# Optimization experiments

Hardware: AMD Instinct MI355X
Metric: run time of the kernel (lower is better)

The kernel has to match this reference:

```python
import jax, jax.numpy as jnp
import numpy as np

D_IN = 1024
D_OUT = 1024
NUM_HEADS = 16
HEAD_DIM = D_OUT // NUM_HEADS


def setup_inputs() -> dict:
    key = jax.random.key(0)
    k_x, k_q, k_k, k_v, k_o, k_ob = jax.random.split(key, 6)
    s_in = 1.0 / np.sqrt(D_IN)
    s_out = 1.0 / np.sqrt(D_OUT)
    return {
        "x": jax.random.normal(k_x, (4, 2048, D_IN), dtype=jnp.float32),
        "W_Q": jax.random.uniform(k_q, (D_IN, D_OUT), jnp.float32, -s_in, s_in),
        "W_K": jax.random.uniform(k_k, (D_IN, D_OUT), jnp.float32, -s_in, s_in),
        "W_V": jax.random.uniform(k_v, (D_IN, D_OUT), jnp.float32, -s_in, s_in),
        "W_O": jax.random.uniform(k_o, (D_OUT, D_OUT), jnp.float32, -s_out, s_out),
        "b_O": jax.random.uniform(k_ob, (D_OUT,), jnp.float32, -s_out, s_out),
    }


def reference(x, W_Q, W_K, W_V, W_O, b_O):
    B, T, _ = x.shape
    # projections -> [B, H, T, Dh]
    Q = (x @ W_Q).reshape(B, T, NUM_HEADS, HEAD_DIM).transpose(0, 2, 1, 3)
    K = (x @ W_K).reshape(B, T, NUM_HEADS, HEAD_DIM).transpose(0, 2, 1, 3)
    V = (x @ W_V).reshape(B, T, NUM_HEADS, HEAD_DIM).transpose(0, 2, 1, 3)
    scores = jnp.einsum("bhqd,bhkd->bhqk", Q, K) / np.sqrt(HEAD_DIM).astype(np.float32)
    causal = jnp.tril(jnp.ones((T, T), dtype=bool))  # True = keep
    scores = jnp.where(causal, scores, -jnp.inf)
    weights = jax.nn.softmax(scores, axis=-1)
    ctx = jnp.einsum("bhqk,bhkd->bhqd", weights, V)
    ctx = ctx.transpose(0, 2, 1, 3).reshape(B, T, D_OUT)
    return ctx @ W_O + b_O
```

## Files before the change

### kernel.cpp

```cpp
#include <hip/hip_runtime.h>

typedef unsigned short ushort_t;
typedef __attribute__((ext_vector_type(8))) __bf16 bf16x8;
typedef __attribute__((ext_vector_type(4))) float f32x4;
typedef __attribute__((ext_vector_type(16))) float f32x16;
typedef __attribute__((ext_vector_type(4))) unsigned short us4;
typedef __attribute__((ext_vector_type(8))) unsigned short us8;
typedef __attribute__((ext_vector_type(4))) unsigned int u32x4;

#define AS1 __attribute__((address_space(1)))
#define AS3 __attribute__((address_space(3)))

__device__ __forceinline__ unsigned short f2bf(float f) {
    unsigned u = __float_as_uint(f);
    u += 0x7fff + ((u >> 16) & 1);
    return (unsigned short)(u >> 16);
}

__device__ __forceinline__ unsigned cvtpk_bf16(float lo, float hi) {
    unsigned r;
    asm("v_cvt_pk_bf16_f32 %0, %1, %2" : "=v"(r) : "v"(lo), "v"(hi));
    return r;
}

__device__ __forceinline__ float fast_exp2(float x) {
    float r;
    asm("v_exp_f32 %0, %1" : "=v"(r) : "v"(x));
    return r;
}

__global__ void k_convert_x(const float* __restrict__ x, ushort_t* __restrict__ xb, int n4) {
    int i = blockIdx.x * blockDim.x + threadIdx.x;
    int stride = gridDim.x * blockDim.x;
    for (; i < n4; i += stride) {
        float4 f = reinterpret_cast<const float4*>(x)[i];
        us4 o = { f2bf(f.x), f2bf(f.y), f2bf(f.z), f2bf(f.w) };
        reinterpret_cast<us4*>(xb)[i] = o;
    }
}

__global__ void k_transpose_w(const float* __restrict__ wq, const float* __restrict__ wk,
                              const float* __restrict__ wv, const float* __restrict__ wo,
                              ushort_t* __restrict__ wqkvt, ushort_t* __restrict__ wot) {
    __shared__ float t[64][65];
    int bx = blockIdx.x;
    int w = bx >> 8;
    int ti = bx & 255;
    int k0 = (ti >> 4) * 64, n0 = (ti & 15) * 64;
    const float* src = (w == 0) ? wq : (w == 1) ? wk : (w == 2) ? wv : wo;
    ushort_t* dst = (w < 3) ? (wqkvt + (size_t)w * 1048576) : wot;
    for (int i = threadIdx.x; i < 4096; i += 256) {
        int r = i >> 6, c = i & 63;
        t[c][r] = src[(size_t)(k0 + r) * 1024 + n0 + c];
    }
    __syncthreads();
    for (int i = threadIdx.x; i < 4096; i += 256) {
        int r = i >> 6, c = i & 63;
        dst[(size_t)(n0 + r) * 1024 + k0 + c] = f2bf(t[r][c]);
    }
}

__global__ __launch_bounds__(512, 2) void k_gemm_qkv256(
    const ushort_t* __restrict__ A, const ushort_t* __restrict__ Bm,
    ushort_t* __restrict__ qd, ushort_t* __restrict__ kd, ushort_t* __restrict__ vd) {
    __shared__ __attribute__((aligned(16))) ushort_t lds[2 * 28672];

    const int tid = threadIdx.x, wid = tid >> 6, lane = tid & 63;
    const int lr = lane & 15, lg = lane >> 4;
    const int wm = wid >> 2, wn = wid & 3;

    int bid = blockIdx.x;
    int wg = (bid & 7) * 64 + (bid >> 3);
    const int by = wg >> 4, bx = wg & 15;
    const int row0 = by * 256, col0 = bx * 192;

    const int srcrow = lane >> 2;
    const int srccol = (((lane & 3) * 16) ^ ((lane >> 5) << 5)) >> 1;
    const ushort_t* aS = A  + (size_t)(row0 + srcrow) * 1024 + srccol;
    const ushort_t* bS = Bm + (size_t)(col0 + srcrow) * 1024 + srccol;
    const int rdoff = (lr * 64 + lg * 16) ^ ((lr >> 3) << 5);

    const int s0 = (wid & 3) + ((wid >> 2) << 3);
    const int s1 = s0 + 4;
    const int bmix_sr = 8 + (wid & 3);
    const int bmix_sc = wid >> 2;

#define STG_A(kt, sr, sc) \
    __builtin_amdgcn_global_load_lds((const AS1 void*)(aS + (size_t)(sr) * 16384 + (kt) * 64 + (sc) * 32), \
        (AS3 void*)((AS3 char*)lds + ((kt) & 1) * 57344 + (sr) * 2048 + (sc) * 1024), 16, 0, 0)
#define STG_B(kt, sr, sc) \
    __builtin_amdgcn_global_load_lds((const AS1 void*)(bS + (size_t)(sr) * 16384 + (kt) * 64 + (sc) * 32), \
        (AS3 void*)((AS3 char*)lds + ((kt) & 1) * 57344 + 32768 + (sr) * 2048 + (sc) * 1024), 16, 0, 0)
#define GRP1(kt)  { STG_A(kt, s0, 0); STG_B(kt, wid, 0); }
#define GRP2(kt)  { STG_A(kt, s1, 0); }
#define GRP3(kt)  { STG_A(kt, s0, 1); STG_B(kt, wid, 1); }
#define GTOP(kt)  { STG_A(kt, s1, 1); STG_B(kt, bmix_sr, bmix_sc); }

    f32x4 acc[8][3] = {};

    GRP1(0); GRP2(0); GRP3(0); GTOP(0);
    GRP1(1); GRP2(1); GRP3(1);

#pragma unroll 1
    for (int kt = 0; kt < 16; ++kt) {
        if (kt < 15) asm volatile("s_waitcnt vmcnt(5)" ::: "memory");
        else         asm volatile("s_waitcnt vmcnt(0)" ::: "memory");
        __builtin_amdgcn_s_barrier();
        if (kt < 15) GTOP(kt + 1);

        const char* bufA = (const char*)lds + (kt & 1) * 57344;
        const char* bufB = bufA + 32768;

        bf16x8 av0[4], av1[4], bv0[3], bv1[3];
#pragma unroll
        for (int x = 0; x < 4; ++x)
            av0[x] = *reinterpret_cast<const bf16x8*>(bufA + (wm * 8 + x) * 2048 + rdoff);
#pragma unroll
        for (int x = 0; x < 3; ++x)
            bv0[x] = *reinterpret_cast<const bf16x8*>(bufB + (wn * 3 + x) * 2048 + rdoff);

#pragma unroll
        for (int x = 0; x < 4; ++x)
            av1[x] = *reinterpret_cast<const bf16x8*>(bufA + (wm * 8 + 4 + x) * 2048 + rdoff);
        __builtin_amdgcn_s_setprio(1);
#pragma unroll
        for (int mf = 0; mf < 4; ++mf)
#pragma unroll
            for (int nf = 0; nf < 3; ++nf)
                acc[mf][nf] = __builtin_amdgcn_mfma_f32_16x16x32_bf16(av0[mf], bv0[nf], acc[mf][nf], 0, 0, 0);
        __builtin_amdgcn_s_setprio(0);
        __builtin_amdgcn_s_barrier();

#pragma unroll
        for (int x = 0; x < 4; ++x)
            av0[x] = *reinterpret_cast<const bf16x8*>(bufA + (wm * 8 + x) * 2048 + 1024 + rdoff);
#pragma unroll
        for (int x = 0; x < 3; ++x)
            bv1[x] = *reinterpret_cast<const bf16x8*>(bufB + (wn * 3 + x) * 2048 + 1024 + rdoff);
        __builtin_amdgcn_s_setprio(1);
#pragma unroll
        for (int mf = 0; mf < 4; ++mf)
#pragma unroll
            for (int nf = 0; nf < 3; ++nf)
                acc[4 + mf][nf] = __builtin_amdgcn_mfma_f32_16x16x32_bf16(av1[mf], bv0[nf], acc[4 + mf][nf], 0, 0, 0);
        __builtin_amdgcn_s_setprio(0);
        if (kt < 14) GRP1(kt + 2);
        __builtin_amdgcn_s_barrier();

#pragma unroll
        for (int x = 0; x < 4; ++x)
            av1[x] = *reinterpret_cast<const bf16x8*>(bufA + (wm * 8 + 4 + x) * 2048 + 1024 + rdoff);
        __builtin_amdgcn_s_setprio(1);
#pragma unroll
        for (int mf = 0; mf < 4; ++mf)
#pragma unroll
            for (int nf = 0; nf < 3; ++nf)
                acc[mf][nf] = __builtin_amdgcn_mfma_f32_16x16x32_bf16(av0[mf], bv1[nf], acc[mf][nf], 0, 0, 0);
        __builtin_amdgcn_s_setprio(0);
        if (kt < 14) GRP2(kt + 2);
        __builtin_amdgcn_s_barrier();

        __builtin_amdgcn_s_setprio(1);
#pragma unroll
        for (int mf = 0; mf < 4; ++mf)
#pragma unroll
            for (int nf = 0; nf < 3; ++nf)
                acc[4 + mf][nf] = __builtin_amdgcn_mfma_f32_16x16x32_bf16(av1[mf], bv1[nf], acc[4 + mf][nf], 0, 0, 0);
        __builtin_amdgcn_s_setprio(0);
        if (kt < 14) GRP3(kt + 2);
    }
#undef STG_A
#undef STG_B
#undef GRP1
#undef GRP2
#undef GRP3
#undef GTOP

#pragma unroll
    for (int mi = 0; mi < 8; ++mi) {
#pragma unroll
        for (int nf = 0; nf < 3; ++nf) {
            int col = col0 + wn * 48 + nf * 16 + lr;
            int w = col >> 10;
            int c1 = col & 1023;
            int h = c1 >> 6, dh = c1 & 63;
            ushort_t* dst = (w == 0) ? qd : (w == 1) ? kd : vd;
            const float osc = (w == 0) ? 0.18033688f : 1.0f;
#pragma unroll
            for (int e = 0; e < 4; ++e) {
                int row = row0 + wm * 128 + mi * 16 + lg * 4 + e;
                int b = row >> 11, t = row & 2047;
                dst[(((size_t)(b * 16 + h)) * 2048 + t) * 64 + dh] = f2bf(acc[mi][nf][e] * osc);
            }
        }
    }
}

__global__ __launch_bounds__(256) void k_transpose_v(const ushort_t* __restrict__ vd,
                                                     ushort_t* __restrict__ vt) {
    __shared__ __attribute__((aligned(16))) ushort_t tile[64 * 72];
    int bid = blockIdx.x;
    int bh = bid >> 5, tt = bid & 31;
    const ushort_t* src = vd + ((size_t)bh * 2048 + tt * 64) * 64;
    ushort_t* dst = vt + (size_t)bh * 2048 * 64 + tt * 64;
#pragma unroll
    for (int r = 0; r < 2; ++r) {
        int i = r * 256 + threadIdx.x;
        int t = i >> 3, c8 = (i & 7) * 8;
        us8 v = *reinterpret_cast<const us8*>(src + (size_t)t * 64 + c8);
        *reinterpret_cast<us8*>(&tile[t * 72 + (c8 ^ ((t >> 3) << 3))]) = v;
    }
    __syncthreads();
#pragma unroll
    for (int r = 0; r < 2; ++r) {
        int i = r * 256 + threadIdx.x;
        int dh = i >> 3, t8 = (i & 7) * 8;
        us8 o;
#pragma unroll
        for (int e = 0; e < 8; ++e)
            o[e] = tile[(t8 + e) * 72 + (dh ^ ((t8 >> 3) << 3))];
        *reinterpret_cast<us8*>(dst + (size_t)dh * 2048 + t8) = o;
    }
}

__global__ __launch_bounds__(256) void k_attn(
    const ushort_t* __restrict__ q, const ushort_t* __restrict__ k,
    const ushort_t* __restrict__ v, ushort_t* __restrict__ ctx) {
    __shared__ __attribute__((aligned(16))) ushort_t lsK[2 * 8192];
    __shared__ __attribute__((aligned(16))) ushort_t lsV[2 * 8192];

    const int tid = threadIdx.x, wid = tid >> 6, lane = tid & 63;
    const int l31 = lane & 31, hi = lane >> 5;
    const int bid = blockIdx.x;
    const int bh = bid >> 3, pi = bid & 7;
    const size_t base = (size_t)bh * 2048 * 64;
    const ushort_t* qg = q + base;
    const ushort_t* kg = k + base;
    const ushort_t* vtg = v + base;
    const int b = bh >> 4, h = bh & 15;

    const int skey = wid * 8 + (lane >> 3);
    const int scb0 = ((lane & 7) * 16) ^ ((skey & 7) << 4);
    const int kx = (l31 & 7) << 4;
    int koffA[4];
#pragma unroll
    for (int s = 0; s < 4; ++s)
        koffA[s] = l31 * 128 + ((s * 32 + hi * 16) ^ kx);

    us8 ow;
#pragma unroll
    for (int e = 0; e < 8; ++e) ow[e] = 0x3F80;
    const bf16x8 onef = __builtin_bit_cast(bf16x8, ow);

#pragma unroll 1
    for (int pass = 0; pass < 2; ++pass) {
        const int qt = pass ? pi : (15 - pi);
        const int q0 = qt * 128;
        const int q0w = q0 + wid * 32;
        const int qrow = q0w + l31;
        const int njt = qt + 1;

        bf16x8 qf[4];
#pragma unroll
        for (int s = 0; s < 4; ++s)
            qf[s] = *reinterpret_cast<const bf16x8*>(qg + (size_t)qrow * 64 + s * 16 + hi * 8);

        const ushort_t* kpr[4];
        const ushort_t* vpr[4];
#pragma unroll
        for (int r = 0; r < 4; ++r) {
            kpr[r] = kg + (size_t)(r * 32 + skey) * 64 + (scb0 >> 1);
            vpr[r] = vtg + (size_t)((r & 1) * 32 + skey) * 2048 + (r >> 1) * 64 + (scb0 >> 1);
        }

        f32x16 acc0 = {}, acc1 = {}, lacc = {};

        __syncthreads();
#pragma unroll
        for (int r = 0; r < 4; ++r) {
            __builtin_amdgcn_global_load_lds((const AS1 void*)kpr[r],
                (AS3 void*)((AS3 char*)lsK + r * 4096 + wid * 1024), 16, 0, 0);
            __builtin_amdgcn_global_load_lds((const AS1 void*)vpr[r],
                (AS3 void*)((AS3 char*)lsV + r * 4096 + wid * 1024), 16, 0, 0);
        }

        unsigned bo = 0;
        for (int jt = 0; jt < njt; ++jt) {
            __syncthreads();
            const int j0 = jt << 7;
            if (jt + 1 < njt) {
                const unsigned nb = bo ^ 16384;
#pragma unroll
                for (int r = 0; r < 4; ++r) {
                    kpr[r] += 8192;
                    vpr[r] += 128;
                    __builtin_amdgcn_global_load_lds((const AS1 void*)kpr[r],
                        (AS3 void*)((AS3 char*)lsK + nb + r * 4096 + wid * 1024), 16, 0, 0);
                    __builtin_amdgcn_global_load_lds((const AS1 void*)vpr[r],
                        (AS3 void*)((AS3 char*)lsV + nb + r * 4096 + wid * 1024), 16, 0, 0);
                }
            }

#pragma unroll
            for (int hh = 0; hh < 2; ++hh) {
                const int j0h = j0 + hh * 64;
                if (j0h < q0w + 32) {
                    const char* bK = reinterpret_cast<const char*>(lsK) + bo + hh * 8192;
                    const char* bV = reinterpret_cast<const char*>(lsV) + bo + hh * 8192;

                    f32x16 s0 = {}, s1 = {};
#pragma unroll
                    for (int s = 0; s < 4; ++s) {
                        bf16x8 ka = *reinterpret_cast<const bf16x8*>(bK + koffA[s]);
                        s0 = __builtin_amdgcn_mfma_f32_32x32x16_bf16(ka, qf[s], s0, 0, 0, 0);
                    }
#pragma unroll
                    for (int s = 0; s < 4; ++s) {
                        bf16x8 ka = *reinterpret_cast<const bf16x8*>(bK + 4096 + koffA[s]);
                        s1 = __builtin_amdgcn_mfma_f32_32x32x16_bf16(ka, qf[s], s1, 0, 0, 0);
                    }

                    float p0[16], p1[16];
                    if (j0h + 63 > q0w) {
                        const int jh = j0h + 4 * hi;
#pragma unroll
                        for (int r = 0; r < 16; ++r) {
                            const int kl = jh + (r & 3) + 8 * (r >> 2);
                            float e0 = fast_exp2(s0[r]);
                            float e1 = fast_exp2(s1[r]);
                            p0[r] = (kl > qrow) ? 0.f : e0;
                            p1[r] = (kl + 32 > qrow) ? 0.f : e1;
                        }
                    } else {
#pragma unroll
                        for (int r = 0; r < 16; ++r) {
                            p0[r] = fast_exp2(s0[r]);
                            p1[r] = fast_exp2(s1[r]);
                        }
                    }

#pragma unroll
                    for (int kb = 0; kb < 2; ++kb) {
                        const float* pp = kb ? p1 : p0;
                        unsigned pw[8];
#pragma unroll
                        for (int g = 0; g < 4; ++g) {
                            pw[2 * g]     = cvtpk_bf16(pp[4 * g],     pp[4 * g + 1]);
                            pw[2 * g + 1] = cvtpk_bf16(pp[4 * g + 2], pp[4 * g + 3]);
                        }
#pragma unroll
                        for (int j = 0; j < 2; ++j) {
                            asm("v_permlane32_swap_b32 %0, %1" : "+v"(pw[4 * j]),     "+v"(pw[4 * j + 2]));
                            asm("v_permlane32_swap_b32 %0, %1" : "+v"(pw[4 * j + 1]), "+v"(pw[4 * j + 3]));
                            u32x4 fw = { pw[4 * j], pw[4 * j + 1], pw[4 * j + 2], pw[4 * j + 3] };
                            bf16x8 pf = __builtin_bit_cast(bf16x8, fw);
                            const int jj = kb * 2 + j;
                            {
                                bf16x8 vf = *reinterpret_cast<const bf16x8*>(bV + koffA[jj]);
                                acc0 = __builtin_amdgcn_mfma_f32_32x32x16_bf16(vf, pf, acc0, 0, 0, 0);
                            }
                            {
                                bf16x8 vf = *reinterpret_cast<const bf16x8*>(bV + 4096 + koffA[jj]);
                                acc1 = __builtin_amdgcn_mfma_f32_32x32x16_bf16(vf, pf, acc1, 0, 0, 0);
                            }
                            lacc = __builtin_amdgcn_mfma_f32_32x32x16_bf16(onef, pf, lacc, 0, 0, 0);
                        }
                    }
                }
            }
            bo ^= 16384;
        }

        float inv = 1.0f / lacc[0];
        size_t orow = ((size_t)(b * 2048 + qrow)) * 1024 + h * 64;
#pragma unroll
        for (int g = 0; g < 4; ++g) {
            us4 o0 = { f2bf(acc0[4 * g] * inv),     f2bf(acc0[4 * g + 1] * inv),
                       f2bf(acc0[4 * g + 2] * inv), f2bf(acc0[4 * g + 3] * inv) };
            *reinterpret_cast<us4*>(&ctx[orow + 8 * g + 4 * hi]) = o0;
            us4 o1 = { f2bf(acc1[4 * g] * inv),     f2bf(acc1[4 * g + 1] * inv),
                       f2bf(acc1[4 * g + 2] * inv), f2bf(acc1[4 * g + 3] * inv) };
            *reinterpret_cast<us4*>(&ctx[orow + 32 + 8 * g + 4 * hi]) = o1;
        }
    }
}

__global__ __launch_bounds__(256) void k_gemm_out(
    const ushort_t* __restrict__ cb, const ushort_t* __restrict__ wot,
    const float* __restrict__ bO, float* __restrict__ out) {
    __shared__ ushort_t lA[128 * 32];
    __shared__ ushort_t lB[128 * 32];
    const int tid = threadIdx.x, wid = tid >> 6, lane = tid & 63;
    const int lr = lane & 15, lg = lane >> 4;
    const int wm = wid >> 1, wn = wid & 1;
    const int bx = blockIdx.x;
    const int by = blockIdx.y;
    const int row0 = by * 128, col0 = bx * 128;
    const int crow = lane >> 2;
    const int coff = (lane & 3) * 8;

    f32x4 acc[4][4] = {};

    for (int k0 = 0; k0 < 1024; k0 += 32) {
        for (int c = wid; c < 8; c += 4) {
            const ushort_t* ga = cb + (size_t)(row0 + c * 16 + crow) * 1024 + k0 + coff;
            __builtin_amdgcn_global_load_lds((const AS1 void*)ga, (AS3 void*)(lA + c * 512), 16, 0, 0);
            const ushort_t* gb = wot + (size_t)(col0 + c * 16 + crow) * 1024 + k0 + coff;
            __builtin_amdgcn_global_load_lds((const AS1 void*)gb, (AS3 void*)(lB + c * 512), 16, 0, 0);
        }
        __syncthreads();
        bf16x8 af[4], bfr[4];
#pragma unroll
        for (int i = 0; i < 4; ++i) {
            af[i]  = *reinterpret_cast<const bf16x8*>(lA + (wm * 64 + i * 16 + lr) * 32 + lg * 8);
            bfr[i] = *reinterpret_cast<const bf16x8*>(lB + (wn * 64 + i * 16 + lr) * 32 + lg * 8);
        }
#pragma unroll
        for (int mi = 0; mi < 4; ++mi)
#pragma unroll
            for (int ni = 0; ni < 4; ++ni)
                acc[mi][ni] = __builtin_amdgcn_mfma_f32_16x16x32_bf16(af[mi], bfr[ni], acc[mi][ni], 0, 0, 0);
        __syncthreads();
    }

#pragma unroll
    for (int mi = 0; mi < 4; ++mi) {
#pragma unroll
        for (int ni = 0; ni < 4; ++ni) {
            int col = col0 + wn * 64 + ni * 16 + lr;
            float bias = bO[col];
#pragma unroll
            for (int e = 0; e < 4; ++e) {
                int row = row0 + wm * 64 + mi * 16 + lg * 4 + e;
                out[(size_t)row * 1024 + col] = acc[mi][ni][e] + bias;
            }
        }
    }
}

extern "C" void kernel_launch(void* const* d_in, const int* in_sizes, int n_in,
                              void* d_out, int out_size, void* d_ws, size_t ws_size,
                              hipStream_t stream) {
    const float* x  = (const float*)d_in[0];
    const float* wq = (const float*)d_in[1];
    const float* wk = (const float*)d_in[2];
    const float* wv = (const float*)d_in[3];
    const float* wo = (const float*)d_in[4];
    const float* bo = (const float*)d_in[5];
    float* out = (float*)d_out;

    char* ws = (char*)d_ws;
    ushort_t* xb    = (ushort_t*)(ws);
    ushort_t* wqkvt = (ushort_t*)(ws + 16777216);
    ushort_t* wot   = (ushort_t*)(ws + 23068672);
    ushort_t* qd    = (ushort_t*)(ws + 25165824);
    ushort_t* kd    = (ushort_t*)(ws + 41943040);
    ushort_t* vd    = (ushort_t*)(ws + 58720256);
    ushort_t* cd    = (ushort_t*)(ws + 75497472);
    ushort_t* vt    = xb;

    k_convert_x<<<2048, 256, 0, stream>>>(x, xb, 8192 * 1024 / 4);
    k_transpose_w<<<1024, 256, 0, stream>>>(wq, wk, wv, wo, wqkvt, wot);
    k_gemm_qkv256<<<512, 512, 0, stream>>>(xb, wqkvt, qd, kd, vd);
    k_transpose_v<<<2048, 256, 0, stream>>>(vd, vt);
    k_attn<<<512, 256, 0, stream>>>(qd, kd, vt, cd);
    k_gemm_out<<<dim3(8, 64), 256, 0, stream>>>(cd, wot, bo, out);
}
```

Before: 168.7 us.

## Pipeline output GEMM with double-buffered swizzled LDS and remap attention block order

Rewrites the output projection GEMM to use a K-tile of 64 with double-buffered LDS, staged global-to-LDS prefetches two tiles ahead, XOR-swizzled LDS layout, and interleaved barriers with MFMA priority bumps. It also remaps the 1D grid so neighbouring blocks share weight columns. Separately, attention blocks are reordered so consecutive blocks cover different heads rather than different query chunks of the same head, which changes load balance for the causal workload. The aim is to hide global-load latency and cut bank conflicts, at the cost of more LDS per block and more complex wait-count bookkeeping.

```diff
diff --git a/kernel.cpp b/kernel.cpp
--- a/kernel.cpp
+++ b/kernel.cpp
@@ -232,7 +232,7 @@
     const int tid = threadIdx.x, wid = tid >> 6, lane = tid & 63;
     const int l31 = lane & 31, hi = lane >> 5;
     const int bid = blockIdx.x;
-    const int bh = bid >> 3, pi = bid & 7;
+    const int bh = bid & 63, pi = bid >> 6;
     const size_t base = (size_t)bh * 2048 * 64;
     const ushort_t* qg = q + base;
     const ushort_t* kg = k + base;
@@ -385,54 +385,120 @@
     }
 }
 
-__global__ __launch_bounds__(256) void k_gemm_out(
+__global__ __launch_bounds__(256, 2) void k_gemm_out(
     const ushort_t* __restrict__ cb, const ushort_t* __restrict__ wot,
     const float* __restrict__ bO, float* __restrict__ out) {
-    __shared__ ushort_t lA[128 * 32];
-    __shared__ ushort_t lB[128 * 32];
+    __shared__ __attribute__((aligned(16))) ushort_t lds[2 * 16384];
+
     const int tid = threadIdx.x, wid = tid >> 6, lane = tid & 63;
     const int lr = lane & 15, lg = lane >> 4;
     const int wm = wid >> 1, wn = wid & 1;
-    const int bx = blockIdx.x;
-    const int by = blockIdx.y;
+
+    int bid = blockIdx.x;
+    int wg = (bid & 7) * 64 + (bid >> 3);
+    const int by = wg >> 3, bx = wg & 7;
     const int row0 = by * 128, col0 = bx * 128;
-    const int crow = lane >> 2;
-    const int coff = (lane & 3) * 8;
+
+    const int srcrow = lane >> 2;
+    const int srccol = (((lane & 3) * 16) ^ ((lane >> 5) << 5)) >> 1;
+    const ushort_t* aS = cb  + (size_t)(row0 + srcrow) * 1024 + srccol;
+    const ushort_t* bS = wot + (size_t)(col0 + srcrow) * 1024 + srccol;
+    const int rdoff = (lr * 64 + lg * 16) ^ ((lr >> 3) << 5);
+
+#define STG_A(kt, sr, sc) \
+    __builtin_amdgcn_global_load_lds((const AS1 void*)(aS + (size_t)(sr) * 16384 + (kt) * 64 + (sc) * 32), \
+        (AS3 void*)((AS3 char*)lds + ((kt) & 1) * 32768 + (sr) * 2048 + (sc) * 1024), 16, 0, 0)
+#define STG_B(kt, sr, sc) \
+    __builtin_amdgcn_global_load_lds((const AS1 void*)(bS + (size_t)(sr) * 16384 + (kt) * 64 + (sc) * 32), \
+        (AS3 void*)((AS3 char*)lds + ((kt) & 1) * 32768 + 16384 + (sr) * 2048 + (sc) * 1024), 16, 0, 0)
+#define GRP1(kt)  { STG_A(kt, wid, 0); STG_A(kt, wid + 4, 0); STG_B(kt, wid, 0); STG_B(kt, wid + 4, 0); }
+#define GTOP(kt)  { STG_A(kt, wid, 1); STG_A(kt, wid + 4, 1); STG_B(kt, wid, 1); STG_B(kt, wid + 4, 1); }
 
     f32x4 acc[4][4] = {};
 
-    for (int k0 = 0; k0 < 1024; k0 += 32) {
-        for (int c = wid; c < 8; c += 4) {
-            const ushort_t* ga = cb + (size_t)(row0 + c * 16 + crow) * 1024 + k0 + coff;
-            __builtin_amdgcn_global_load_lds((const AS1 void*)ga, (AS3 void*)(lA + c * 512), 16, 0, 0);
-            const ushort_t* gb = wot + (size_t)(col0 + c * 16 + crow) * 1024 + k0 + coff;
-            __builtin_amdgcn_global_load_lds((const AS1 void*)gb, (AS3 void*)(lB + c * 512), 16, 0, 0);
-        }
-        __syncthreads();
-        bf16x8 af[4], bfr[4];
-#pragma unroll
-        for (int i = 0; i < 4; ++i) {
-            af[i]  = *reinterpret_cast<const bf16x8*>(lA + (wm * 64 + i * 16 + lr) * 32 + lg * 8);
-            bfr[i] = *reinterpret_cast<const bf16x8*>(lB + (wn * 64 + i * 16 + lr) * 32 + lg * 8);
-        }
-#pragma unroll
-        for (int mi = 0; mi < 4; ++mi)
-#pragma unroll
-            for (int ni = 0; ni < 4; ++ni)
-                acc[mi][ni] = __builtin_amdgcn_mfma_f32_16x16x32_bf16(af[mi], bfr[ni], acc[mi][ni], 0, 0, 0);
-        __syncthreads();
-    }
-
-#pragma unroll
-    for (int mi = 0; mi < 4; ++mi) {
-#pragma unroll
-        for (int ni = 0; ni < 4; ++ni) {
-            int col = col0 + wn * 64 + ni * 16 + lr;
+    GRP1(0); GTOP(0); GRP1(1);
+
+#pragma unroll 1
+    for (int kt = 0; kt < 16; ++kt) {
+        if (kt < 15) asm volatile("s_waitcnt vmcnt(4)" ::: "memory");
+        else         asm volatile("s_waitcnt vmcnt(0)" ::: "memory");
+        __builtin_amdgcn_s_barrier();
+        if (kt < 15) GTOP(kt + 1);
+
+        const char* bufA = (const char*)lds + (kt & 1) * 32768;
+        const char* bufB = bufA + 16384;
+
+        bf16x8 av0[2], av1[2], bv0[4], bv1[4];
+#pragma unroll
+        for (int x = 0; x < 2; ++x)
+            av0[x] = *reinterpret_cast<const bf16x8*>(bufA + (wm * 4 + x) * 2048 + rdoff);
+#pragma unroll
+        for (int x = 0; x < 4; ++x)
+            bv0[x] = *reinterpret_cast<const bf16x8*>(bufB + (wn * 4 + x) * 2048 + rdoff);
+
+#pragma unroll
+        for (int x = 0; x < 2; ++x)
+            av1[x] = *reinterpret_cast<const bf16x8*>(bufA + (wm * 4 + 2 + x) * 2048 + rdoff);
+        __builtin_amdgcn_s_setprio(1);
+#pragma unroll
+        for (int mf = 0; mf < 2; ++mf)
+#pragma unroll
+            for (int nf = 0; nf < 4; ++nf)
+                acc[mf][nf] = __builtin_amdgcn_mfma_f32_16x16x32_bf16(av0[mf], bv0[nf], acc[mf][nf], 0, 0, 0);
+        __builtin_amdgcn_s_setprio(0);
+        __builtin_amdgcn_s_barrier();
+
+#pragma unroll
+        for (int x = 0; x < 2; ++x)
+            av0[x] = *reinterpret_cast<const bf16x8*>(bufA + (wm * 4 + x) * 2048 + 1024 + rdoff);
+#pragma unroll
+        for (int x = 0; x < 4; ++x)
+            bv1[x] = *reinterpret_cast<const bf16x8*>(bufB + (wn * 4 + x) * 2048 + 1024 + rdoff);
+        __builtin_amdgcn_s_setprio(1);
+#pragma unroll
+        for (int mf = 0; mf < 2; ++mf)
+#pragma unroll
+            for (int nf = 0; nf < 4; ++nf)
+                acc[2 + mf][nf] = __builtin_amdgcn_mfma_f32_16x16x32_bf16(av1[mf], bv0[nf], acc[2 + mf][nf], 0, 0, 0);
+        __builtin_amdgcn_s_setprio(0);
+        if (kt < 14) GRP1(kt + 2);
+        __builtin_amdgcn_s_barrier();
+
+#pragma unroll
+        for (int x = 0; x < 2; ++x)
+            av1[x] = *reinterpret_cast<const bf16x8*>(bufA + (wm * 4 + 2 + x) * 2048 + 1024 + rdoff);
+        __builtin_amdgcn_s_setprio(1);
+#pragma unroll
+        for (int mf = 0; mf < 2; ++mf)
+#pragma unroll
+            for (int nf = 0; nf < 4; ++nf)
+                acc[mf][nf] = __builtin_amdgcn_mfma_f32_16x16x32_bf16(av0[mf], bv1[nf], acc[mf][nf], 0, 0, 0);
+        __builtin_amdgcn_s_setprio(0);
+        __builtin_amdgcn_s_barrier();
+
+        __builtin_amdgcn_s_setprio(1);
+#pragma unroll
+        for (int mf = 0; mf < 2; ++mf)
+#pragma unroll
+            for (int nf = 0; nf < 4; ++nf)
+                acc[2 + mf][nf] = __builtin_amdgcn_mfma_f32_16x16x32_bf16(av1[mf], bv1[nf], acc[2 + mf][nf], 0, 0, 0);
+        __builtin_amdgcn_s_setprio(0);
+    }
+#undef STG_A
+#undef STG_B
+#undef GRP1
+#undef GTOP
+
+#pragma unroll
+    for (int mf = 0; mf < 4; ++mf) {
+#pragma unroll
+        for (int nf = 0; nf < 4; ++nf) {
+            int col = col0 + wn * 64 + nf * 16 + lr;
             float bias = bO[col];
 #pragma unroll
             for (int e = 0; e < 4; ++e) {
-                int row = row0 + wm * 64 + mi * 16 + lg * 4 + e;
-                out[(size_t)row * 1024 + col] = acc[mi][ni][e] + bias;
+                int row = row0 + wm * 64 + mf * 16 + lg * 4 + e;
+                out[(size_t)row * 1024 + col] = acc[mf][nf][e] + bias;
             }
         }
     }
@@ -464,5 +530,5 @@
     k_gemm_qkv256<<<512, 512, 0, stream>>>(xb, wqkvt, qd, kd, vd);
     k_transpose_v<<<2048, 256, 0, stream>>>(vd, vt);
     k_attn<<<512, 256, 0, stream>>>(qd, kd, vt, cd);
-    k_gemm_out<<<dim3(8, 64), 256, 0, stream>>>(cd, wot, bo, out);
-}
+    k_gemm_out<<<dim3(512), 256, 0, stream>>>(cd, wot, bo, out);
+}
```

New measurement: 156.8 us. -7.1%, faster.
